# Kernel optimization log

Measured on AMD Instinct MI355X. Metric: run time of the kernel, lower is better.

## Reference

```python
import jax, jax.numpy as jnp
import numpy as np


def setup_inputs() -> dict:
    key = jax.random.key(0)
    W = jax.random.normal(key, (64, 16, 128, 128), dtype=jnp.float32)
    return {"W": W, "num_iters": 5}


def reference(W, num_iters):
    """Newton-Schulz iterative matrix inverse: X_{k+1} = X_k (2I - W X_k).

    Init: X_0 = W^T / (||W||_1 * ||W||_inf), the classical convergent start.
    W: [..., N, N] batched square matrices.
    """
    n = W.shape[-1]
    absW = jnp.abs(W)
    norm1 = jnp.max(jnp.sum(absW, axis=-2), axis=-1)    # max abs column sum
    norminf = jnp.max(jnp.sum(absW, axis=-1), axis=-1)  # max abs row sum
    scale = (norm1 * norminf)[..., None, None]
    X = jnp.swapaxes(W, -1, -2) / scale
    two_I = 2.0 * jnp.eye(n, dtype=W.dtype)
    for _ in range(num_iters):
        X = jnp.matmul(X, two_I - jnp.matmul(W, X))
    return X
```

## Files before the change

kernel.cpp:

```cpp
#include <hip/hip_runtime.h>


#define NN 128

typedef __attribute__((ext_vector_type(8))) short bf16x8;
typedef __attribute__((ext_vector_type(16))) float f32x16;
typedef __attribute__((ext_vector_type(4))) float f32x4;
typedef __attribute__((ext_vector_type(4))) unsigned short us4;

#define XRM_OFF 0
#define XCM_OFF 32768
#define RED_OFF 65536
#define LDS_BYTES 66560

__device__ __forceinline__ unsigned short f2bf(float f) {
  unsigned u = __float_as_uint(f);
  return (unsigned short)((u + 0x7FFFu + ((u >> 16) & 1u)) >> 16);
}
__device__ __forceinline__ float bf2f(unsigned short h) {
  return __uint_as_float(((unsigned)h) << 16);
}
__device__ __forceinline__ f32x16 zero16() {
  f32x16 z;
#pragma unroll
  for (int i = 0; i < 16; ++i) z[i] = 0.0f;
  return z;
}
__device__ __forceinline__ int swz8(int R, int k0) {
  return R * 128 + (((k0 >> 3) ^ (R & 7)) << 3);
}
__device__ __forceinline__ int swz4(int R, int c0) {
  return R * 128 + ((((c0 >> 3) ^ (R & 7)) << 3) | (c0 & 7));
}
__device__ __forceinline__ int swz1(int R, int c) {
  return R * 128 + ((((c >> 3) ^ (R & 7)) << 3) | (c & 7));
}

__global__ void __launch_bounds__(512, 4)
ns_inverse_kernel(const float* __restrict__ Wglob, const int* __restrict__ nIt,
                  float* __restrict__ outglob) {
  extern __shared__ char lds[];
  unsigned short* xrm = (unsigned short*)(lds + XRM_OFF);
  unsigned short* xcm = (unsigned short*)(lds + XCM_OFF);
  float* red   = (float*)(lds + RED_OFF);
  float* stage = (float*)lds;

  const int b = blockIdx.x;
  const float* Wg = Wglob + (size_t)b * (NN * NN);
  float* outg = outglob + (size_t)b * (NN * NN);
  const int t = threadIdx.x;
  const int lane = t & 63;
  const int wv = t >> 6;
  const int l31 = lane & 31;
  const int half = lane >> 5;
  const int s = wv & 3;
  const int u = wv >> 2;
  const int niters = nIt[0];

  {
    const f32x4* src = (const f32x4*)Wg;
    f32x4* dst = (f32x4*)stage;
#pragma unroll
    for (int i = 0; i < 8; ++i) dst[t + 512 * i] = src[t + 512 * i];
  }
  __syncthreads();

  if (t < 128) {
    float ssum = 0.f;
    for (int jj = 0; jj < NN; ++jj) { int j = (jj + t) & 127; ssum += fabsf(stage[t * NN + j]); }
    red[t] = ssum;
  } else if (t < 256) {
    int c = t - 128;
    float ssum = 0.f;
    for (int i = 0; i < NN; ++i) ssum += fabsf(stage[i * NN + c]);
    red[128 + c] = ssum;
  }
  __syncthreads();
  float ninf = 0.f, n1 = 0.f;
  for (int i = 0; i < 128; ++i) {
    ninf = fmaxf(ninf, red[i]);
    n1   = fmaxf(n1,   red[128 + i]);
  }
  const float scale = 1.0f / (n1 * ninf);

  bf16x8 wfrag[8];
  {
    const int am = 32 * s + l31;
#pragma unroll
    for (int ks = 0; ks < 8; ++ks) {
      const float* p = stage + am * NN + ks * 16 + half * 8;
      f32x4 a = *(const f32x4*)p;
      f32x4 bq = *(const f32x4*)(p + 4);
      bf16x8 f;
      f[0] = (short)f2bf(a[0]);  f[1] = (short)f2bf(a[1]);
      f[2] = (short)f2bf(a[2]);  f[3] = (short)f2bf(a[3]);
      f[4] = (short)f2bf(bq[0]); f[5] = (short)f2bf(bq[1]);
      f[6] = (short)f2bf(bq[2]); f[7] = (short)f2bf(bq[3]);
      wfrag[ks] = f;
    }
  }
  __syncthreads();

#pragma unroll
  for (int i = 0; i < 8; ++i) {
    int e0 = (t + 512 * i) * 4;
    int R = e0 >> 7, c0 = e0 & 127;
    f32x4 v = *(const f32x4*)(Wg + e0);
    us4 h4;
#pragma unroll
    for (int j = 0; j < 4; ++j) h4[j] = f2bf(v[j] * scale);
    *(us4*)(xcm + swz4(R, c0)) = h4;
  }
  {
    const int r = t & 127;
    const int kc = (t >> 7) * 32;
#pragma unroll
    for (int j4 = 0; j4 < 8; ++j4) {
      int c0 = kc + j4 * 4;
      us4 h4;
#pragma unroll
      for (int i = 0; i < 4; ++i) h4[i] = f2bf(Wg[(size_t)(c0 + i) * NN + r] * scale);
      *(us4*)(xrm + swz4(r, c0)) = h4;
    }
  }
  __syncthreads();

  const int pX = 32 * s + l31;
  const int rr = 32 * u + l31;
  for (int it = 0; it < niters; ++it) {
    const bool last = (it == niters - 1);

    {
      f32x16 t0 = zero16();
#pragma unroll
      for (int ks = 0; ks < 8; ++ks) {
        bf16x8 bv = *(const bf16x8*)(xcm + swz8(rr, ks * 16 + half * 8));
        t0 = __builtin_amdgcn_mfma_f32_32x32x16_bf16(wfrag[ks], bv, t0, 0, 0, 0);
      }
      __syncthreads();
#pragma unroll
      for (int q = 0; q < 4; ++q) {
        us4 h4;
#pragma unroll
        for (int i = 0; i < 4; ++i) h4[i] = f2bf(t0[4 * q + i]);
        *(us4*)(xcm + swz4(rr, 32 * s + 8 * q + 4 * half)) = h4;
      }
    }
    {
      f32x16 t1 = zero16();
#pragma unroll
      for (int ks = 0; ks < 8; ++ks) {
        bf16x8 bv = *(const bf16x8*)(xcm + swz8(64 + rr, ks * 16 + half * 8));
        t1 = __builtin_amdgcn_mfma_f32_32x32x16_bf16(wfrag[ks], bv, t1, 0, 0, 0);
      }
      __syncthreads();
#pragma unroll
      for (int q = 0; q < 4; ++q) {
        us4 h4;
#pragma unroll
        for (int i = 0; i < 4; ++i) h4[i] = f2bf(t1[4 * q + i]);
        *(us4*)(xcm + 64 * 128 + swz4(rr, 32 * s + 8 * q + 4 * half)) = h4;
      }
    }

    f32x16 acc0 = zero16();
#pragma unroll
    for (int ks = 0; ks < 8; ++ks) {
      int k0 = ks * 16 + half * 8;
      bf16x8 av = *(const bf16x8*)(xcm + swz8(rr, k0));
      bf16x8 bv = *(const bf16x8*)(xrm + swz8(pX, k0));
      acc0 = __builtin_amdgcn_mfma_f32_32x32x16_bf16(av, bv, acc0, 0, 0, 0);
    }
    __syncthreads();

    f32x16 acc1 = zero16();
#pragma unroll
    for (int ks = 0; ks < 8; ++ks) {
      int k0 = ks * 16 + half * 8;
      bf16x8 av = *(const bf16x8*)(xcm + 64 * 128 + swz8(rr, k0));
      bf16x8 bv = *(const bf16x8*)(xrm + swz8(pX, k0));
      acc1 = __builtin_amdgcn_mfma_f32_32x32x16_bf16(av, bv, acc1, 0, 0, 0);
    }
    __syncthreads();

#pragma unroll
    for (int c = 0; c < 2; ++c) {
      const f32x16 ac = c ? acc1 : acc0;
#pragma unroll
      for (int q = 0; q < 4; ++q) {
        int c0m = 64 * c + 32 * u + 8 * q + 4 * half;
        int offr = swz4(pX, c0m);
        us4 xh4 = *(const us4*)(xrm + offr);
        f32x4 v;
#pragma unroll
        for (int i = 0; i < 4; ++i)
          v[i] = 2.0f * bf2f(xh4[i]) - ac[4 * q + i];
        if (last) {
          *(f32x4*)(outg + pX * NN + c0m) = v;
        } else {
          us4 h4;
#pragma unroll
          for (int i = 0; i < 4; ++i) {
            unsigned short hh = f2bf(v[i]);
            h4[i] = hh;
            xcm[swz1(c0m + i, pX)] = hh;
          }
          *(us4*)(xrm + offr) = h4;
        }
      }
    }
    __syncthreads();
  }
}

extern "C" void kernel_launch(void* const* d_in, const int* in_sizes, int n_in,
                              void* d_out, int out_size, void* d_ws, size_t ws_size,
                              hipStream_t stream) {
  const float* W = (const float*)d_in[0];
  const int* nIt = (const int*)d_in[1];
  float* out = (float*)d_out;
  const int nmat = in_sizes[0] / (NN * NN);

  hipFuncSetAttribute((const void*)ns_inverse_kernel,
                      hipFuncAttributeMaxDynamicSharedMemorySize, LDS_BYTES);
  ns_inverse_kernel<<<nmat, 512, LDS_BYTES, stream>>>(W, nIt, out);
}
```

Baseline: 208.2 us.

## Use 1024-thread blocks with one 32x32 tile per wave and separate staging LDS

Doubles the block to 16 waves so each wave computes a single 32x32 output tile per GEMM instead of two. This removes the duplicated half-matrix passes and one barrier stage per iteration. Initial X construction now reads W from the LDS staging buffer instead of re-reading global memory, which is why the staging area gets its own region. LDS use roughly doubles to about 129 KB per block, which limits residency to one block per CU and cuts latency hiding across blocks.

After: 253.5 us. 21.8% more time.

```diff
diff --git a/kernel.cpp b/kernel.cpp
--- a/kernel.cpp
+++ b/kernel.cpp
@@ -8,10 +8,11 @@
 typedef __attribute__((ext_vector_type(4))) float f32x4;
 typedef __attribute__((ext_vector_type(4))) unsigned short us4;
 
-#define XRM_OFF 0
-#define XCM_OFF 32768
-#define RED_OFF 65536
-#define LDS_BYTES 66560
+#define STAGE_OFF 0
+#define XRM_OFF   65536
+#define XCM_OFF   98304
+#define RED_OFF   131072
+#define LDS_BYTES 132096
 
 __device__ __forceinline__ unsigned short f2bf(float f) {
   unsigned u = __float_as_uint(f);
@@ -36,14 +37,14 @@
   return R * 128 + ((((c >> 3) ^ (R & 7)) << 3) | (c & 7));
 }
 
-__global__ void __launch_bounds__(512, 4)
+__global__ void __launch_bounds__(1024, 4)
 ns_inverse_kernel(const float* __restrict__ Wglob, const int* __restrict__ nIt,
                   float* __restrict__ outglob) {
   extern __shared__ char lds[];
+  float* stage = (float*)(lds + STAGE_OFF);
   unsigned short* xrm = (unsigned short*)(lds + XRM_OFF);
   unsigned short* xcm = (unsigned short*)(lds + XCM_OFF);
-  float* red   = (float*)(lds + RED_OFF);
-  float* stage = (float*)lds;
+  float* red = (float*)(lds + RED_OFF);
 
   const int b = blockIdx.x;
   const float* Wg = Wglob + (size_t)b * (NN * NN);
@@ -54,14 +55,14 @@
   const int l31 = lane & 31;
   const int half = lane >> 5;
   const int s = wv & 3;
-  const int u = wv >> 2;
+  const int v = wv >> 2;
   const int niters = nIt[0];
 
   {
     const f32x4* src = (const f32x4*)Wg;
     f32x4* dst = (f32x4*)stage;
 #pragma unroll
-    for (int i = 0; i < 8; ++i) dst[t + 512 * i] = src[t + 512 * i];
+    for (int i = 0; i < 4; ++i) dst[t + 1024 * i] = src[t + 1024 * i];
   }
   __syncthreads();
 
@@ -99,114 +100,84 @@
       wfrag[ks] = f;
     }
   }
-  __syncthreads();
 
 #pragma unroll
-  for (int i = 0; i < 8; ++i) {
-    int e0 = (t + 512 * i) * 4;
+  for (int i = 0; i < 4; ++i) {
+    int e0 = (t + 1024 * i) * 4;
     int R = e0 >> 7, c0 = e0 & 127;
-    f32x4 v = *(const f32x4*)(Wg + e0);
+    f32x4 vv = *(const f32x4*)(stage + e0);
     us4 h4;
 #pragma unroll
-    for (int j = 0; j < 4; ++j) h4[j] = f2bf(v[j] * scale);
+    for (int j = 0; j < 4; ++j) h4[j] = f2bf(vv[j] * scale);
     *(us4*)(xcm + swz4(R, c0)) = h4;
   }
   {
     const int r = t & 127;
-    const int kc = (t >> 7) * 32;
+    const int kc = (t >> 7) * 16;
 #pragma unroll
-    for (int j4 = 0; j4 < 8; ++j4) {
+    for (int j4 = 0; j4 < 4; ++j4) {
       int c0 = kc + j4 * 4;
       us4 h4;
 #pragma unroll
-      for (int i = 0; i < 4; ++i) h4[i] = f2bf(Wg[(size_t)(c0 + i) * NN + r] * scale);
+      for (int i = 0; i < 4; ++i) h4[i] = f2bf(stage[(c0 + i) * NN + r] * scale);
       *(us4*)(xrm + swz4(r, c0)) = h4;
     }
   }
   __syncthreads();
 
   const int pX = 32 * s + l31;
-  const int rr = 32 * u + l31;
+  const int rv = 32 * v + l31;
   for (int it = 0; it < niters; ++it) {
     const bool last = (it == niters - 1);
 
     {
-      f32x16 t0 = zero16();
+      f32x16 tt = zero16();
 #pragma unroll
       for (int ks = 0; ks < 8; ++ks) {
-        bf16x8 bv = *(const bf16x8*)(xcm + swz8(rr, ks * 16 + half * 8));
-        t0 = __builtin_amdgcn_mfma_f32_32x32x16_bf16(wfrag[ks], bv, t0, 0, 0, 0);
+        bf16x8 bv = *(const bf16x8*)(xcm + swz8(rv, ks * 16 + half * 8));
+        tt = __builtin_amdgcn_mfma_f32_32x32x16_bf16(wfrag[ks], bv, tt, 0, 0, 0);
       }
       __syncthreads();
 #pragma unroll
       for (int q = 0; q < 4; ++q) {
         us4 h4;
 #pragma unroll
-        for (int i = 0; i < 4; ++i) h4[i] = f2bf(t0[4 * q + i]);
-        *(us4*)(xcm + swz4(rr, 32 * s + 8 * q + 4 * half)) = h4;
+        for (int i = 0; i < 4; ++i) h4[i] = f2bf(tt[4 * q + i]);
+        *(us4*)(xcm + swz4(rv, 32 * s + 8 * q + 4 * half)) = h4;
       }
     }
-    {
-      f32x16 t1 = zero16();
-#pragma unroll
-      for (int ks = 0; ks < 8; ++ks) {
-        bf16x8 bv = *(const bf16x8*)(xcm + swz8(64 + rr, ks * 16 + half * 8));
-        t1 = __builtin_amdgcn_mfma_f32_32x32x16_bf16(wfrag[ks], bv, t1, 0, 0, 0);
-      }
-      __syncthreads();
-#pragma unroll
-      for (int q = 0; q < 4; ++q) {
-        us4 h4;
-#pragma unroll
-        for (int i = 0; i < 4; ++i) h4[i] = f2bf(t1[4 * q + i]);
-        *(us4*)(xcm + 64 * 128 + swz4(rr, 32 * s + 8 * q + 4 * half)) = h4;
-      }
-    }
+    __syncthreads();
 
-    f32x16 acc0 = zero16();
+    f32x16 acc = zero16();
 #pragma unroll
     for (int ks = 0; ks < 8; ++ks) {
       int k0 = ks * 16 + half * 8;
-      bf16x8 av = *(const bf16x8*)(xcm + swz8(rr, k0));
-      bf16x8 bv = *(const bf16x8*)(xrm + swz8(pX, k0));
-      acc0 = __builtin_amdgcn_mfma_f32_32x32x16_bf16(av, bv, acc0, 0, 0, 0);
-    }
-    __syncthreads();
-
-    f32x16 acc1 = zero16();
-#pragma unroll
-    for (int ks = 0; ks < 8; ++ks) {
-      int k0 = ks * 16 + half * 8;
-      bf16x8 av = *(const bf16x8*)(xcm + 64 * 128 + swz8(rr, k0));
-      bf16x8 bv = *(const bf16x8*)(xrm + swz8(pX, k0));
-      acc1 = __builtin_amdgcn_mfma_f32_32x32x16_bf16(av, bv, acc1, 0, 0, 0);
+      bf16x8 av  = *(const bf16x8*)(xcm + swz8(rv, k0));
+      bf16x8 bvv = *(const bf16x8*)(xrm + swz8(pX, k0));
+      acc = __builtin_amdgcn_mfma_f32_32x32x16_bf16(av, bvv, acc, 0, 0, 0);
     }
     __syncthreads();
 
 #pragma unroll
-    for (int c = 0; c < 2; ++c) {
-      const f32x16 ac = c ? acc1 : acc0;
+    for (int q = 0; q < 4; ++q) {
+      int c0m = 32 * v + 8 * q + 4 * half;
+      int offr = swz4(pX, c0m);
+      us4 xh4 = *(const us4*)(xrm + offr);
+      f32x4 vv;
 #pragma unroll
-      for (int q = 0; q < 4; ++q) {
-        int c0m = 64 * c + 32 * u + 8 * q + 4 * half;
-        int offr = swz4(pX, c0m);
-        us4 xh4 = *(const us4*)(xrm + offr);
-        f32x4 v;
+      for (int i = 0; i < 4; ++i)
+        vv[i] = 2.0f * bf2f(xh4[i]) - acc[4 * q + i];
+      if (last) {
+        *(f32x4*)(outg + pX * NN + c0m) = vv;
+      } else {
+        us4 h4;
 #pragma unroll
-        for (int i = 0; i < 4; ++i)
-          v[i] = 2.0f * bf2f(xh4[i]) - ac[4 * q + i];
-        if (last) {
-          *(f32x4*)(outg + pX * NN + c0m) = v;
-        } else {
-          us4 h4;
-#pragma unroll
-          for (int i = 0; i < 4; ++i) {
-            unsigned short hh = f2bf(v[i]);
-            h4[i] = hh;
-            xcm[swz1(c0m + i, pX)] = hh;
-          }
-          *(us4*)(xrm + offr) = h4;
+        for (int i = 0; i < 4; ++i) {
+          unsigned short hh = f2bf(vv[i]);
+          h4[i] = hh;
+          xcm[swz1(c0m + i, pX)] = hh;
         }
+        *(us4*)(xrm + offr) = h4;
       }
     }
     __syncthreads();
@@ -223,5 +194,5 @@
 
   hipFuncSetAttribute((const void*)ns_inverse_kernel,
                       hipFuncAttributeMaxDynamicSharedMemorySize, LDS_BYTES);
-  ns_inverse_kernel<<<nmat, 512, LDS_BYTES, stream>>>(W, nIt, out);
+  ns_inverse_kernel<<<nmat, 1024, LDS_BYTES, stream>>>(W, nIt, out);
 }
```

## Spill W fragments to global scratch and merge second-stage GEMMs into one pass

Applied to the files above, without the earlier changes.

Stops holding the bf16 W MFMA fragments in registers. They are written once to a global scratch buffer (the workspace, or the output buffer as a fallback) and reloaded each iteration, which cuts VGPR pressure and may raise occupancy. The two X·(W X) GEMM passes are merged into one loop in which each wave computes two 32x32 tiles sharing the same B fragment, removing one barrier and halving the B reloads. The cost is extra global or L2 traffic on every iteration, and the fallback scratch aliases the output buffer while the last iteration writes to it.

Result: slower. 217.1 us (+4.3%).

```diff
diff --git a/kernel.cpp b/kernel.cpp
--- a/kernel.cpp
+++ b/kernel.cpp
@@ -38,7 +38,7 @@
 
 __global__ void __launch_bounds__(512, 4)
 ns_inverse_kernel(const float* __restrict__ Wglob, const int* __restrict__ nIt,
-                  float* __restrict__ outglob) {
+                  float* outglob, unsigned short* fragbase, int fragstride) {
   extern __shared__ char lds[];
   unsigned short* xrm = (unsigned short*)(lds + XRM_OFF);
   unsigned short* xcm = (unsigned short*)(lds + XCM_OFF);
@@ -48,6 +48,7 @@
   const int b = blockIdx.x;
   const float* Wg = Wglob + (size_t)b * (NN * NN);
   float* outg = outglob + (size_t)b * (NN * NN);
+  unsigned short* frag = fragbase + (size_t)b * fragstride;
   const int t = threadIdx.x;
   const int lane = t & 63;
   const int wv = t >> 6;
@@ -83,21 +84,20 @@
   }
   const float scale = 1.0f / (n1 * ninf);
 
-  bf16x8 wfrag[8];
-  {
-    const int am = 32 * s + l31;
-#pragma unroll
-    for (int ks = 0; ks < 8; ++ks) {
-      const float* p = stage + am * NN + ks * 16 + half * 8;
-      f32x4 a = *(const f32x4*)p;
-      f32x4 bq = *(const f32x4*)(p + 4);
-      bf16x8 f;
-      f[0] = (short)f2bf(a[0]);  f[1] = (short)f2bf(a[1]);
-      f[2] = (short)f2bf(a[2]);  f[3] = (short)f2bf(a[3]);
-      f[4] = (short)f2bf(bq[0]); f[5] = (short)f2bf(bq[1]);
-      f[6] = (short)f2bf(bq[2]); f[7] = (short)f2bf(bq[3]);
-      wfrag[ks] = f;
-    }
+#pragma unroll
+  for (int j = 0; j < 4; ++j) {
+    int idx = t * 4 + j;
+    int sfr = idx >> 9, ks = (idx >> 6) & 7, ln = idx & 63;
+    int am = 32 * sfr + (ln & 31);
+    int k0 = 16 * ks + 8 * (ln >> 5);
+    const float* p = stage + am * NN + k0;
+    f32x4 a = *(const f32x4*)p, bq = *(const f32x4*)(p + 4);
+    bf16x8 f;
+    f[0] = (short)f2bf(a[0]);  f[1] = (short)f2bf(a[1]);
+    f[2] = (short)f2bf(a[2]);  f[3] = (short)f2bf(a[3]);
+    f[4] = (short)f2bf(bq[0]); f[5] = (short)f2bf(bq[1]);
+    f[6] = (short)f2bf(bq[2]); f[7] = (short)f2bf(bq[3]);
+    *(bf16x8*)(frag + (size_t)idx * 8) = f;
   }
   __syncthreads();
 
@@ -134,8 +134,9 @@
       f32x16 t0 = zero16();
 #pragma unroll
       for (int ks = 0; ks < 8; ++ks) {
+        bf16x8 av = *(const bf16x8*)(frag + (size_t)((s * 8 + ks) * 64 + lane) * 8);
         bf16x8 bv = *(const bf16x8*)(xcm + swz8(rr, ks * 16 + half * 8));
-        t0 = __builtin_amdgcn_mfma_f32_32x32x16_bf16(wfrag[ks], bv, t0, 0, 0, 0);
+        t0 = __builtin_amdgcn_mfma_f32_32x32x16_bf16(av, bv, t0, 0, 0, 0);
       }
       __syncthreads();
 #pragma unroll
@@ -150,8 +151,9 @@
       f32x16 t1 = zero16();
 #pragma unroll
       for (int ks = 0; ks < 8; ++ks) {
+        bf16x8 av = *(const bf16x8*)(frag + (size_t)((s * 8 + ks) * 64 + lane) * 8);
         bf16x8 bv = *(const bf16x8*)(xcm + swz8(64 + rr, ks * 16 + half * 8));
-        t1 = __builtin_amdgcn_mfma_f32_32x32x16_bf16(wfrag[ks], bv, t1, 0, 0, 0);
+        t1 = __builtin_amdgcn_mfma_f32_32x32x16_bf16(av, bv, t1, 0, 0, 0);
       }
       __syncthreads();
 #pragma unroll
@@ -162,46 +164,39 @@
         *(us4*)(xcm + 64 * 128 + swz4(rr, 32 * s + 8 * q + 4 * half)) = h4;
       }
     }
-
-    f32x16 acc0 = zero16();
+    __syncthreads();
+
+    f32x16 a0 = zero16(), a1 = zero16();
 #pragma unroll
     for (int ks = 0; ks < 8; ++ks) {
       int k0 = ks * 16 + half * 8;
-      bf16x8 av = *(const bf16x8*)(xcm + swz8(rr, k0));
-      bf16x8 bv = *(const bf16x8*)(xrm + swz8(pX, k0));
-      acc0 = __builtin_amdgcn_mfma_f32_32x32x16_bf16(av, bv, acc0, 0, 0, 0);
+      bf16x8 bv  = *(const bf16x8*)(xrm + swz8(pX, k0));
+      bf16x8 av0 = *(const bf16x8*)(xcm + swz8(64 * u + l31, k0));
+      bf16x8 av1 = *(const bf16x8*)(xcm + swz8(64 * u + 32 + l31, k0));
+      a0 = __builtin_amdgcn_mfma_f32_32x32x16_bf16(av0, bv, a0, 0, 0, 0);
+      a1 = __builtin_amdgcn_mfma_f32_32x32x16_bf16(av1, bv, a1, 0, 0, 0);
     }
     __syncthreads();
 
-    f32x16 acc1 = zero16();
-#pragma unroll
-    for (int ks = 0; ks < 8; ++ks) {
-      int k0 = ks * 16 + half * 8;
-      bf16x8 av = *(const bf16x8*)(xcm + 64 * 128 + swz8(rr, k0));
-      bf16x8 bv = *(const bf16x8*)(xrm + swz8(pX, k0));
-      acc1 = __builtin_amdgcn_mfma_f32_32x32x16_bf16(av, bv, acc1, 0, 0, 0);
-    }
-    __syncthreads();
-
-#pragma unroll
-    for (int c = 0; c < 2; ++c) {
-      const f32x16 ac = c ? acc1 : acc0;
+#pragma unroll
+    for (int j = 0; j < 2; ++j) {
+      const f32x16 ac = j ? a1 : a0;
 #pragma unroll
       for (int q = 0; q < 4; ++q) {
-        int c0m = 64 * c + 32 * u + 8 * q + 4 * half;
+        int c0m = 32 * (2 * u + j) + 8 * q + 4 * half;
         int offr = swz4(pX, c0m);
         us4 xh4 = *(const us4*)(xrm + offr);
-        f32x4 v;
+        f32x4 vv;
 #pragma unroll
         for (int i = 0; i < 4; ++i)
-          v[i] = 2.0f * bf2f(xh4[i]) - ac[4 * q + i];
+          vv[i] = 2.0f * bf2f(xh4[i]) - ac[4 * q + i];
         if (last) {
-          *(f32x4*)(outg + pX * NN + c0m) = v;
+          *(f32x4*)(outg + pX * NN + c0m) = vv;
         } else {
           us4 h4;
 #pragma unroll
           for (int i = 0; i < 4; ++i) {
-            unsigned short hh = f2bf(v[i]);
+            unsigned short hh = f2bf(vv[i]);
             h4[i] = hh;
             xcm[swz1(c0m + i, pX)] = hh;
           }
@@ -221,7 +216,17 @@
   float* out = (float*)d_out;
   const int nmat = in_sizes[0] / (NN * NN);
 
+  unsigned short* fragbase;
+  int fragstride;
+  if (ws_size >= (size_t)nmat * NN * NN * sizeof(unsigned short)) {
+    fragbase = (unsigned short*)d_ws;
+    fragstride = NN * NN;
+  } else {
+    fragbase = (unsigned short*)d_out;
+    fragstride = NN * NN * 2;
+  }
+
   hipFuncSetAttribute((const void*)ns_inverse_kernel,
                       hipFuncAttributeMaxDynamicSharedMemorySize, LDS_BYTES);
-  ns_inverse_kernel<<<nmat, 512, LDS_BYTES, stream>>>(W, nIt, out);
-}
+  ns_inverse_kernel<<<nmat, 512, LDS_BYTES, stream>>>(W, nIt, out, fragbase, fragstride);
+}
```
